# Kernel optimization log

Hardware: AMD Instinct MI355X
Metric: run time of the kernel (lower is better)

## Reference

```python
import jax, jax.numpy as jnp
import numpy as np

N = 100000      # nodes
E = 1600000     # edges (avg degree 16)
EP = 500000     # pos/neg scored edges
DIN, DH, DOUT = 128, 128, 64


def setup_inputs() -> dict:
    key = jax.random.key(0)
    ks = jax.random.split(key, 8)
    x = jax.random.normal(ks[0], (N, DIN), jnp.float32)
    edge_index = jax.random.randint(ks[1], (2, E), 0, N)
    pos_edge_index = jax.random.randint(ks[2], (2, EP), 0, N)
    neg_edge_index = jax.random.randint(ks[3], (2, EP), 0, N)
    s = lambda k, sh: jax.random.normal(k, sh, jnp.float32) * 0.05
    return dict(
        x=x, edge_index=edge_index,
        pos_edge_index=pos_edge_index, neg_edge_index=neg_edge_index,
        W_l0=s(ks[4], (DIN, DH)), b_l0=jnp.zeros((DH,), jnp.float32), W_r0=s(ks[5], (DIN, DH)),
        W_l1=s(ks[6], (DH, DOUT)), b_l1=jnp.zeros((DOUT,), jnp.float32), W_r1=s(ks[7], (DH, DOUT)),
    )


def sage_conv(h, src, dst, W_l, b_l, W_r):
    # PyG SAGEConv (mean aggr): out_i = W_l @ mean_{j in N(i)} h_j + b_l + W_r @ h_i
    msg = h[src]                                                   # [E, d] gather
    agg = jax.ops.segment_sum(msg, dst, num_segments=h.shape[0])   # [N, d]
    deg = jax.ops.segment_sum(jnp.ones((src.shape[0],), h.dtype), dst, num_segments=h.shape[0])
    mean = agg / jnp.maximum(deg, 1.0)[:, None]
    return mean @ W_l + b_l + h @ W_r


def reference(x, edge_index, pos_edge_index, neg_edge_index,
              W_l0, b_l0, W_r0, W_l1, b_l1, W_r1):
    src, dst = edge_index[0], edge_index[1]
    h = sage_conv(x, src, dst, W_l0, b_l0, W_r0)
    h = jax.nn.relu(h)          # dropout is identity in eval mode
    h = sage_conv(h, src, dst, W_l1, b_l1, W_r1)
    pos_scores = (h[pos_edge_index[0]] * h[pos_edge_index[1]]).sum(axis=1)
    neg_scores = (h[neg_edge_index[0]] * h[neg_edge_index[1]]).sum(axis=1)
    return (pos_scores, neg_scores)
```

## Files before the change

kernel.cpp:

```cpp
#include <hip/hip_runtime.h>

#define NN 100000
#define EE 1600000
#define EPE 500000
#define NBINS 196
#define BCAP 12288
#define EPB 2048
#define NB1 782

typedef short bf8_t __attribute__((ext_vector_type(8)));
typedef float f4_t  __attribute__((ext_vector_type(4)));
typedef float f2v  __attribute__((ext_vector_type(2)));

__device__ __forceinline__ unsigned short f2bf(float f) {
    unsigned u = __float_as_uint(f);
    unsigned r = (u + 0x7fffu + ((u >> 16) & 1u)) >> 16;
    return (unsigned short)r;
}
__device__ __forceinline__ float bfl(unsigned u) { return __uint_as_float(u << 16); }
__device__ __forceinline__ float bfh(unsigned u) { return __uint_as_float(u & 0xffff0000u); }

#if __has_builtin(__builtin_amdgcn_cvt_pk_fp8_f32) && __has_builtin(__builtin_amdgcn_cvt_pk_f32_fp8)
__device__ __forceinline__ unsigned pk4_fp8(float a0, float a1, float a2, float a3) {
    int w = 0;
    w = __builtin_amdgcn_cvt_pk_fp8_f32(a0, a1, w, false);
    w = __builtin_amdgcn_cvt_pk_fp8_f32(a2, a3, w, true);
    return (unsigned)w;
}
__device__ __forceinline__ void accf8(float* a, uint2 v) {
    f2v p0 = __builtin_amdgcn_cvt_pk_f32_fp8((int)v.x, false);
    f2v p1 = __builtin_amdgcn_cvt_pk_f32_fp8((int)v.x, true);
    f2v p2 = __builtin_amdgcn_cvt_pk_f32_fp8((int)v.y, false);
    f2v p3 = __builtin_amdgcn_cvt_pk_f32_fp8((int)v.y, true);
    a[0] += p0.x; a[1] += p0.y; a[2] += p1.x; a[3] += p1.y;
    a[4] += p2.x; a[5] += p2.y; a[6] += p3.x; a[7] += p3.y;
}
#else
#include <hip/hip_fp8.h>
__device__ __forceinline__ unsigned pk4_fp8(float a0, float a1, float a2, float a3) {
    unsigned r;
    r  = (unsigned)__hip_cvt_float_to_fp8(a0, __HIP_SATFINITE, __HIP_E4M3);
    r |= (unsigned)__hip_cvt_float_to_fp8(a1, __HIP_SATFINITE, __HIP_E4M3) << 8;
    r |= (unsigned)__hip_cvt_float_to_fp8(a2, __HIP_SATFINITE, __HIP_E4M3) << 16;
    r |= (unsigned)__hip_cvt_float_to_fp8(a3, __HIP_SATFINITE, __HIP_E4M3) << 24;
    return r;
}
__device__ __forceinline__ float dec1_fp8(unsigned b) {
    __hip_fp8_e4m3 h; h.__x = (__hip_fp8_storage_t)(b & 0xff);
    return (float)h;
}
__device__ __forceinline__ void accf8(float* a, uint2 v) {
    a[0] += dec1_fp8(v.x); a[1] += dec1_fp8(v.x >> 8);
    a[2] += dec1_fp8(v.x >> 16); a[3] += dec1_fp8(v.x >> 24);
    a[4] += dec1_fp8(v.y); a[5] += dec1_fp8(v.y >> 8);
    a[6] += dec1_fp8(v.y >> 16); a[7] += dec1_fp8(v.y >> 24);
}
#endif

__global__ __launch_bounds__(256) void binpass1_k(
    const int* __restrict__ src, const int* __restrict__ dst,
    int* __restrict__ bin_cnt, int* __restrict__ binbuf)
{
    __shared__ int cnt_l[NBINS];
    __shared__ int base_l[NBINS];
    int tid = threadIdx.x;
    int e0 = blockIdx.x * EPB;
    for (int i = tid; i < NBINS; i += 256) cnt_l[i] = 0;
    __syncthreads();

    int pk[8];
    #pragma unroll
    for (int i = 0; i < 8; ++i) {
        int e = e0 + tid + i * 256;
        pk[i] = -1;
        if (e < EE) {
            int d = dst[e];
            int b = d >> 9;
            int r = atomicAdd(&cnt_l[b], 1);
            pk[i] = (b << 20) | ((d & 511) << 11) | r;
        }
    }
    __syncthreads();
    for (int i = tid; i < NBINS; i += 256)
        base_l[i] = atomicAdd(&bin_cnt[i], cnt_l[i]);
    __syncthreads();

    #pragma unroll
    for (int i = 0; i < 8; ++i) {
        int e = e0 + tid + i * 256;
        if (e >= EE) continue;
        int v = pk[i];
        int b = v >> 20, dl = (v >> 11) & 511, r = v & 2047;
        binbuf[b * BCAP + base_l[b] + r] = (dl << 17) | src[e];
    }
}

__global__ __launch_bounds__(256) void binpass2_k(
    const int* __restrict__ binbuf, const int* __restrict__ bin_cnt,
    int* __restrict__ csr, int* __restrict__ row_ptr, float* __restrict__ invd)
{
    __shared__ int deg_l[512];
    __shared__ int off_l[512];
    __shared__ int cur_l[512];
    __shared__ int s[256];
    int tid = threadIdx.x;
    int b = blockIdx.x;
    int lo = b << 9;
    int n_here = min(512, NN - lo);

    int bc = (tid < NBINS) ? bin_cnt[tid] : 0;
    s[tid] = bc;
    __syncthreads();
    #pragma unroll
    for (int off = 1; off < 256; off <<= 1) {
        int t = (tid >= off) ? s[tid - off] : 0;
        __syncthreads();
        s[tid] += t;
        __syncthreads();
    }
    int base = (b == 0) ? 0 : s[b - 1];
    int cnt = bin_cnt[b];
    const int* bb = binbuf + b * BCAP;
    __syncthreads();

    deg_l[tid] = 0; deg_l[tid + 256] = 0;
    __syncthreads();
    for (int i = tid; i < cnt; i += 256)
        atomicAdd(&deg_l[bb[i] >> 17], 1);
    __syncthreads();

    int a0 = deg_l[2 * tid], a1 = deg_l[2 * tid + 1];
    s[tid] = a0 + a1;
    __syncthreads();
    #pragma unroll
    for (int off = 1; off < 256; off <<= 1) {
        int t = (tid >= off) ? s[tid - off] : 0;
        __syncthreads();
        s[tid] += t;
        __syncthreads();
    }
    int excl = s[tid] - (a0 + a1);
    off_l[2 * tid] = excl;
    off_l[2 * tid + 1] = excl + a0;
    cur_l[2 * tid] = excl;
    cur_l[2 * tid + 1] = excl + a0;
    __syncthreads();

    for (int j = tid; j < n_here; j += 256) {
        row_ptr[lo + j] = base + off_l[j];
        invd[lo + j] = 1.0f / fmaxf((float)deg_l[j], 1.0f);
    }
    if (tid == 0 && b == NBINS - 1) row_ptr[NN] = EE;

    for (int i = tid; i < cnt; i += 256) {
        int v = bb[i];
        int dstl = v >> 17, srcv = v & 0x1FFFF;
        int pos = atomicAdd(&cur_l[dstl], 1);
        csr[base + pos] = srcv;
    }
}

__global__ void pack_k(const float* __restrict__ Wl0, const float* __restrict__ Wr0,
                       const float* __restrict__ Wl1, const float* __restrict__ Wr1,
                       const float* __restrict__ bl0, const float* __restrict__ bl1,
                       unsigned short* __restrict__ Bp0, unsigned short* __restrict__ Bp1,
                       float* __restrict__ b0p, float* __restrict__ b1p,
                       int* __restrict__ bin_cnt)
{
    int t = blockIdx.x * 256 + threadIdx.x;
    if (t < NBINS) bin_cnt[t] = 0;
    if (t < 4096) {
        int q = t & 3;
        int n = (t >> 2) & 255;
        int kt = t >> 10;
        unsigned short o[8];
        #pragma unroll
        for (int j = 0; j < 8; ++j) {
            int k = kt * 32 + q * 8 + j;
            float v = (n < 128) ? Wl0[(size_t)k * 128 + n] : Wr0[(size_t)k * 128 + (n - 128)];
            o[j] = f2bf(v);
        }
        uint4 w;
        w.x = (unsigned)o[0] | ((unsigned)o[1] << 16);
        w.y = (unsigned)o[2] | ((unsigned)o[3] << 16);
        w.z = (unsigned)o[4] | ((unsigned)o[5] << 16);
        w.w = (unsigned)o[6] | ((unsigned)o[7] << 16);
        *(uint4*)(Bp0 + (size_t)t * 8) = w;
    } else if (t < 6144) {
        int u = t - 4096;
        int q = u & 3;
        int n = (u >> 2) & 127;
        int kt = u >> 9;
        unsigned short o[8];
        #pragma unroll
        for (int j = 0; j < 8; ++j) {
            int k = kt * 32 + q * 8 + j;
            int c = ((k & 7) << 4) | (k >> 3);
            float v = (n < 64) ? Wl1[(size_t)c * 64 + n] : Wr1[(size_t)c * 64 + (n - 64)];
            o[j] = f2bf(v);
        }
        uint4 w;
        w.x = (unsigned)o[0] | ((unsigned)o[1] << 16);
        w.y = (unsigned)o[2] | ((unsigned)o[3] << 16);
        w.z = (unsigned)o[4] | ((unsigned)o[5] << 16);
        w.w = (unsigned)o[6] | ((unsigned)o[7] << 16);
        *(uint4*)(Bp1 + (size_t)u * 8) = w;
    } else if (t < 6144 + 128) {
        int m = t - 6144;
        b0p[m] = bl0[((m & 7) << 4) | (m >> 3)];
    } else if (t < 6144 + 192) {
        int m = t - 6272;
        b1p[m] = bl1[((m & 3) << 4) | (m >> 2)];
    }
}

template<int NCOLS, bool AFP32>
__global__ __launch_bounds__(256) void gemm_k(
    const void* __restrict__ Av, const unsigned short* __restrict__ Bp,
    unsigned char* __restrict__ Tout, unsigned short* __restrict__ Rout)
{
    constexpr int NT = NCOLS / 16;
    constexpr int NTH = NCOLS / 32;
    constexpr int HC = NCOLS / 2;
    int wave = threadIdx.x >> 6;
    int lane = threadIdx.x & 63;
    int ln = lane & 15, q = lane >> 4;
    int row0 = (blockIdx.x * 4 + wave) * 16;
    if (row0 >= NN) return;
    int arow = row0 + ln;

    f4_t acc[NT];
    #pragma unroll
    for (int nt = 0; nt < NT; ++nt) acc[nt] = (f4_t){0.f, 0.f, 0.f, 0.f};

    #pragma unroll
    for (int kt = 0; kt < 4; ++kt) {
        bf8_t a;
        if (AFP32) {
            const float* ap = (const float*)Av + (size_t)arow * 128 + kt * 32 + q * 8;
            f4_t a0 = *(const f4_t*)ap;
            f4_t a1 = *(const f4_t*)(ap + 4);
            #pragma unroll
            for (int j = 0; j < 4; ++j) {
                a[j]     = (short)f2bf(a0[j]);
                a[4 + j] = (short)f2bf(a1[j]);
            }
        } else {
            a = *(const bf8_t*)((const unsigned short*)Av + (size_t)arow * 128 + kt * 32 + q * 8);
        }
        const unsigned short* bb = Bp + (size_t)kt * NCOLS * 32 + (size_t)ln * 32 + q * 8;
        #pragma unroll
        for (int nt = 0; nt < NT; ++nt) {
            bf8_t b = *(const bf8_t*)(bb + nt * 512);
            acc[nt] = __builtin_amdgcn_mfma_f32_16x16x32_bf16(a, b, acc[nt], 0, 0, 0);
        }
    }

    #pragma unroll
    for (int r = 0; r < 4; ++r) {
        int row = row0 + q * 4 + r;
        if (NTH == 8) {
            uint2 wt;
            wt.x = pk4_fp8(acc[0][r], acc[1][r], acc[2][r], acc[3][r]);
            wt.y = pk4_fp8(acc[4][r], acc[5][r], acc[6][r], acc[7][r]);
            *(uint2*)(Tout + (size_t)row * HC + ln * 8) = wt;
            uint4 wr;
            wr.x = (unsigned)f2bf(acc[8][r])  | ((unsigned)f2bf(acc[9][r])  << 16);
            wr.y = (unsigned)f2bf(acc[10][r]) | ((unsigned)f2bf(acc[11][r]) << 16);
            wr.z = (unsigned)f2bf(acc[12][r]) | ((unsigned)f2bf(acc[13][r]) << 16);
            wr.w = (unsigned)f2bf(acc[14][r]) | ((unsigned)f2bf(acc[15][r]) << 16);
            *(uint4*)(Rout + (size_t)row * HC + ln * 8) = wr;
        } else {
            unsigned wt = pk4_fp8(acc[0][r], acc[1][r], acc[2][r], acc[3][r]);
            *(unsigned*)(Tout + (size_t)row * HC + ln * 4) = wt;
            uint2 wr;
            wr.x = (unsigned)f2bf(acc[4][r]) | ((unsigned)f2bf(acc[5][r]) << 16);
            wr.y = (unsigned)f2bf(acc[6][r]) | ((unsigned)f2bf(acc[7][r]) << 16);
            *(uint2*)(Rout + (size_t)row * HC + ln * 4) = wr;
        }
    }
}

__device__ __forceinline__ void unp8(float* a, uint4 v) {
    a[0] = bfl(v.x); a[1] = bfh(v.x);
    a[2] = bfl(v.y); a[3] = bfh(v.y);
    a[4] = bfl(v.z); a[5] = bfh(v.z);
    a[6] = bfl(v.w); a[7] = bfh(v.w);
}

template<int LPNS, bool RELU>
__global__ __launch_bounds__(256) void gather_fuse_k(
    const unsigned char* __restrict__ tq, const int* __restrict__ csr,
    const int* __restrict__ row_ptr, const float* __restrict__ invd,
    const unsigned short* __restrict__ rg, const float* __restrict__ biasp,
    unsigned short* __restrict__ hout)
{
    constexpr int STRIDE = 8 << LPNS;
    int t = blockIdx.x * 256 + threadIdx.x;
    int node = t >> LPNS;
    int lane = t & ((1 << LPNS) - 1);
    if (node >= NN) return;
    int e = row_ptr[node];
    int e1 = row_ptr[node + 1];
    const unsigned char* fb = tq + lane * 8;

    float a0[8] = {0.f, 0.f, 0.f, 0.f, 0.f, 0.f, 0.f, 0.f};
    float a1[8] = {0.f, 0.f, 0.f, 0.f, 0.f, 0.f, 0.f, 0.f};
    for (; e + 3 < e1; e += 4) {
        int s0 = csr[e], s1 = csr[e + 1], s2 = csr[e + 2], s3 = csr[e + 3];
        uint2 v0 = *(const uint2*)(fb + (size_t)s0 * STRIDE);
        uint2 v1 = *(const uint2*)(fb + (size_t)s1 * STRIDE);
        uint2 v2 = *(const uint2*)(fb + (size_t)s2 * STRIDE);
        uint2 v3 = *(const uint2*)(fb + (size_t)s3 * STRIDE);
        accf8(a0, v0); accf8(a1, v1); accf8(a0, v2); accf8(a1, v3);
    }
    for (; e < e1; ++e) {
        int s0 = csr[e];
        uint2 v0 = *(const uint2*)(fb + (size_t)s0 * STRIDE);
        accf8(a0, v0);
    }

    float inv = invd[node];
    uint4 rv = *(const uint4*)(rg + (size_t)node * STRIDE + lane * 8);
    float rr[8];
    unp8(rr, rv);
    f4_t b0 = *(const f4_t*)(biasp + lane * 8);
    f4_t b1 = *(const f4_t*)(biasp + lane * 8 + 4);
    float o[8];
    #pragma unroll
    for (int j = 0; j < 8; ++j) {
        float bj = (j < 4) ? b0[j] : b1[j - 4];
        float v = (a0[j] + a1[j]) * inv + rr[j] + bj;
        o[j] = RELU ? fmaxf(v, 0.f) : v;
    }
    uint4 w;
    w.x = (unsigned)f2bf(o[0]) | ((unsigned)f2bf(o[1]) << 16);
    w.y = (unsigned)f2bf(o[2]) | ((unsigned)f2bf(o[3]) << 16);
    w.z = (unsigned)f2bf(o[4]) | ((unsigned)f2bf(o[5]) << 16);
    w.w = (unsigned)f2bf(o[6]) | ((unsigned)f2bf(o[7]) << 16);
    *(uint4*)(hout + (size_t)node * STRIDE + lane * 8) = w;
}

__device__ __forceinline__ float dot8(uint4 va, uint4 vb) {
    return bfl(va.x) * bfl(vb.x) + bfh(va.x) * bfh(vb.x)
         + bfl(va.y) * bfl(vb.y) + bfh(va.y) * bfh(vb.y)
         + bfl(va.z) * bfl(vb.z) + bfh(va.z) * bfh(vb.z)
         + bfl(va.w) * bfl(vb.w) + bfh(va.w) * bfh(vb.w);
}

__global__ __launch_bounds__(256) void score_k(
    const unsigned short* __restrict__ h2b, const int* __restrict__ pos,
    const int* __restrict__ neg, float* __restrict__ out)
{
    int t = blockIdx.x * 256 + threadIdx.x;
    int g = t >> 3, l = t & 7;
    int eg0 = g * 2;
    if (eg0 >= 2 * EPE) return;
    int eg1 = eg0 + 1;
    int a0i, b0i, a1i, b1i;
    if (eg0 < EPE) { a0i = pos[eg0]; b0i = pos[EPE + eg0]; }
    else { int e2 = eg0 - EPE; a0i = neg[e2]; b0i = neg[EPE + e2]; }
    if (eg1 < EPE) { a1i = pos[eg1]; b1i = pos[EPE + eg1]; }
    else { int e2 = eg1 - EPE; a1i = neg[e2]; b1i = neg[EPE + e2]; }
    const unsigned short* hb = h2b + (size_t)l * 8;
    uint4 va0 = *(const uint4*)(hb + (size_t)a0i * 64);
    uint4 vb0 = *(const uint4*)(hb + (size_t)b0i * 64);
    uint4 va1 = *(const uint4*)(hb + (size_t)a1i * 64);
    uint4 vb1 = *(const uint4*)(hb + (size_t)b1i * 64);
    float p0 = dot8(va0, vb0);
    float p1 = dot8(va1, vb1);
    p0 += __shfl_xor(p0, 1, 8);
    p1 += __shfl_xor(p1, 1, 8);
    p0 += __shfl_xor(p0, 2, 8);
    p1 += __shfl_xor(p1, 2, 8);
    p0 += __shfl_xor(p0, 4, 8);
    p1 += __shfl_xor(p1, 4, 8);
    if (l == 0) { out[eg0] = p0; out[eg1] = p1; }
}

extern "C" void kernel_launch(void* const* d_in, const int* in_sizes, int n_in,
                              void* d_out, int out_size, void* d_ws, size_t ws_size,
                              hipStream_t stream) {
    const float* x   = (const float*)d_in[0];
    const int*   ei  = (const int*)d_in[1];
    const int*   pei = (const int*)d_in[2];
    const int*   nei = (const int*)d_in[3];
    const float* Wl0 = (const float*)d_in[4];
    const float* bl0 = (const float*)d_in[5];
    const float* Wr0 = (const float*)d_in[6];
    const float* Wl1 = (const float*)d_in[7];
    const float* bl1 = (const float*)d_in[8];
    const float* Wr1 = (const float*)d_in[9];
    float* out = (float*)d_out;

    char* ws = (char*)d_ws;
    size_t off = 0;
    auto alloc = [&](size_t bytes) {
        void* p = ws + off;
        off = (off + bytes + 255) & ~(size_t)255;
        return p;
    };
    float* invd     = (float*)alloc((size_t)NN * 4);
    int*   row_ptr  = (int*)  alloc((size_t)(NN + 1) * 4);
    int*   bin_cnt  = (int*)  alloc((size_t)NBINS * 4);
    int*   binbuf   = (int*)  alloc((size_t)NBINS * BCAP * 4);
    int*   csr      = (int*)  alloc((size_t)EE * 4);
    unsigned short* Bp0 = (unsigned short*)alloc((size_t)4096 * 8 * 2);
    unsigned short* Bp1 = (unsigned short*)alloc((size_t)2048 * 8 * 2);
    float* b0p = (float*)alloc(128 * 4);
    float* b1p = (float*)alloc(64 * 4);
    unsigned char*  t0q = (unsigned char*) alloc((size_t)NN * 128);
    unsigned short* r0b = (unsigned short*)alloc((size_t)NN * 128 * 2);
    unsigned short* h1b = (unsigned short*)alloc((size_t)NN * 128 * 2);
    unsigned char*  t1q = t0q;
    unsigned short* r1b = r0b;
    unsigned short* h2b = h1b;

    const int* src = ei;
    const int* dst = ei + EE;

    pack_k<<<25, 256, 0, stream>>>(Wl0, Wr0, Wl1, Wr1, bl0, bl1, Bp0, Bp1, b0p, b1p, bin_cnt);
    binpass1_k<<<NB1, 256, 0, stream>>>(src, dst, bin_cnt, binbuf);
    binpass2_k<<<NBINS, 256, 0, stream>>>(binbuf, bin_cnt, csr, row_ptr, invd);

    gemm_k<256, true><<<1563, 256, 0, stream>>>(x, Bp0, t0q, r0b);
    gather_fuse_k<4, true><<<(NN * 16 + 255) / 256, 256, 0, stream>>>(
        t0q, csr, row_ptr, invd, r0b, b0p, h1b);

    gemm_k<128, false><<<1563, 256, 0, stream>>>(h1b, Bp1, t1q, r1b);
    gather_fuse_k<3, false><<<(NN * 8 + 255) / 256, 256, 0, stream>>>(
        t1q, csr, row_ptr, invd, r1b, b1p, h2b);

    score_k<<<(EPE * 8 + 255) / 256, 256, 0, stream>>>(h2b, pei, nei, out);
}
```

Baseline: 299.0 us.

## Split GEMM columns across waves and keep B fragments in registers

The GEMM now gives each wave a column strip of the output and has it loop over four 16-row tiles, with the B fragments loaded into registers once per block. Before, each wave covered all columns for its own 16 rows and reloaded B for every tile. The column permutation used for the layer-1 weights and the biases is changed to match the new output layout, and a 2-wide fp8 pack is added. In exchange, each A row is now loaded by all four waves instead of one, and the change is only correct if the downstream gather kernel's layout assumptions still hold.

```diff
diff --git a/kernel.cpp b/kernel.cpp
--- a/kernel.cpp
+++ b/kernel.cpp
@@ -20,12 +20,23 @@
 __device__ __forceinline__ float bfl(unsigned u) { return __uint_as_float(u << 16); }
 __device__ __forceinline__ float bfh(unsigned u) { return __uint_as_float(u & 0xffff0000u); }
 
+__device__ __forceinline__ int c0p(int m) {
+    return ((m >> 6) & 1) * 64 + (m & 3) * 16 + ((m >> 2) & 15);
+}
+__device__ __forceinline__ int c1p(int m) {
+    return ((m >> 5) & 1) * 32 + (m & 1) * 16 + ((m >> 1) & 15);
+}
+
 #if __has_builtin(__builtin_amdgcn_cvt_pk_fp8_f32) && __has_builtin(__builtin_amdgcn_cvt_pk_f32_fp8)
 __device__ __forceinline__ unsigned pk4_fp8(float a0, float a1, float a2, float a3) {
     int w = 0;
     w = __builtin_amdgcn_cvt_pk_fp8_f32(a0, a1, w, false);
     w = __builtin_amdgcn_cvt_pk_fp8_f32(a2, a3, w, true);
     return (unsigned)w;
+}
+__device__ __forceinline__ unsigned short pk2_fp8(float a0, float a1) {
+    int w = __builtin_amdgcn_cvt_pk_fp8_f32(a0, a1, 0, false);
+    return (unsigned short)(w & 0xffff);
 }
 __device__ __forceinline__ void accf8(float* a, uint2 v) {
     f2v p0 = __builtin_amdgcn_cvt_pk_f32_fp8((int)v.x, false);
@@ -44,6 +55,12 @@
     r |= (unsigned)__hip_cvt_float_to_fp8(a2, __HIP_SATFINITE, __HIP_E4M3) << 16;
     r |= (unsigned)__hip_cvt_float_to_fp8(a3, __HIP_SATFINITE, __HIP_E4M3) << 24;
     return r;
+}
+__device__ __forceinline__ unsigned short pk2_fp8(float a0, float a1) {
+    unsigned r;
+    r  = (unsigned)__hip_cvt_float_to_fp8(a0, __HIP_SATFINITE, __HIP_E4M3);
+    r |= (unsigned)__hip_cvt_float_to_fp8(a1, __HIP_SATFINITE, __HIP_E4M3) << 8;
+    return (unsigned short)r;
 }
 __device__ __forceinline__ float dec1_fp8(unsigned b) {
     __hip_fp8_e4m3 h; h.__x = (__hip_fp8_storage_t)(b & 0xff);
@@ -195,7 +212,7 @@
         #pragma unroll
         for (int j = 0; j < 8; ++j) {
             int k = kt * 32 + q * 8 + j;
-            int c = ((k & 7) << 4) | (k >> 3);
+            int c = c0p(k);
             float v = (n < 64) ? Wl1[(size_t)c * 64 + n] : Wr1[(size_t)c * 64 + (n - 64)];
             o[j] = f2bf(v);
         }
@@ -207,10 +224,10 @@
         *(uint4*)(Bp1 + (size_t)u * 8) = w;
     } else if (t < 6144 + 128) {
         int m = t - 6144;
-        b0p[m] = bl0[((m & 7) << 4) | (m >> 3)];
+        b0p[m] = bl0[c0p(m)];
     } else if (t < 6144 + 192) {
         int m = t - 6272;
-        b1p[m] = bl1[((m & 3) << 4) | (m >> 2)];
+        b1p[m] = bl1[c1p(m)];
     }
 }
 
@@ -219,64 +236,80 @@
     const void* __restrict__ Av, const unsigned short* __restrict__ Bp,
     unsigned char* __restrict__ Tout, unsigned short* __restrict__ Rout)
 {
-    constexpr int NT = NCOLS / 16;
-    constexpr int NTH = NCOLS / 32;
+    constexpr int STRIP = NCOLS / 4;
+    constexpr int NT = STRIP / 16;
     constexpr int HC = NCOLS / 2;
-    int wave = threadIdx.x >> 6;
+    int w = threadIdx.x >> 6;
     int lane = threadIdx.x & 63;
     int ln = lane & 15, q = lane >> 4;
-    int row0 = (blockIdx.x * 4 + wave) * 16;
-    if (row0 >= NN) return;
-    int arow = row0 + ln;
-
-    f4_t acc[NT];
-    #pragma unroll
-    for (int nt = 0; nt < NT; ++nt) acc[nt] = (f4_t){0.f, 0.f, 0.f, 0.f};
-
-    #pragma unroll
-    for (int kt = 0; kt < 4; ++kt) {
-        bf8_t a;
+    int half = w >> 1, wsub = w & 1;
+    int row0 = blockIdx.x * 64;
+    int colbase = half * HC + wsub * STRIP;
+
+    bf8_t Bf[4][NT];
+    #pragma unroll
+    for (int kt = 0; kt < 4; ++kt)
+        #pragma unroll
+        for (int nt = 0; nt < NT; ++nt)
+            Bf[kt][nt] = *(const bf8_t*)(Bp + (size_t)kt * NCOLS * 32
+                                         + (size_t)(colbase + nt * 16 + ln) * 32 + q * 8);
+
+    for (int rt = 0; rt < 4; ++rt) {
+        int rowt = row0 + rt * 16;
+        if (rowt >= NN) break;
+        int arow = rowt + ln;
+
+        bf8_t Af[4];
         if (AFP32) {
-            const float* ap = (const float*)Av + (size_t)arow * 128 + kt * 32 + q * 8;
-            f4_t a0 = *(const f4_t*)ap;
-            f4_t a1 = *(const f4_t*)(ap + 4);
             #pragma unroll
-            for (int j = 0; j < 4; ++j) {
-                a[j]     = (short)f2bf(a0[j]);
-                a[4 + j] = (short)f2bf(a1[j]);
+            for (int kt = 0; kt < 4; ++kt) {
+                const float* ap = (const float*)Av + (size_t)arow * 128 + kt * 32 + q * 8;
+                f4_t a0 = *(const f4_t*)ap;
+                f4_t a1 = *(const f4_t*)(ap + 4);
+                #pragma unroll
+                for (int j = 0; j < 4; ++j) {
+                    Af[kt][j]     = (short)f2bf(a0[j]);
+                    Af[kt][4 + j] = (short)f2bf(a1[j]);
+                }
             }
         } else {
-            a = *(const bf8_t*)((const unsigned short*)Av + (size_t)arow * 128 + kt * 32 + q * 8);
+            #pragma unroll
+            for (int kt = 0; kt < 4; ++kt)
+                Af[kt] = *(const bf8_t*)((const unsigned short*)Av
+                                         + (size_t)arow * 128 + kt * 32 + q * 8);
         }
-        const unsigned short* bb = Bp + (size_t)kt * NCOLS * 32 + (size_t)ln * 32 + q * 8;
-        #pragma unroll
-        for (int nt = 0; nt < NT; ++nt) {
-            bf8_t b = *(const bf8_t*)(bb + nt * 512);
-            acc[nt] = __builtin_amdgcn_mfma_f32_16x16x32_bf16(a, b, acc[nt], 0, 0, 0);
-        }
-    }
-
-    #pragma unroll
-    for (int r = 0; r < 4; ++r) {
-        int row = row0 + q * 4 + r;
-        if (NTH == 8) {
-            uint2 wt;
-            wt.x = pk4_fp8(acc[0][r], acc[1][r], acc[2][r], acc[3][r]);
-            wt.y = pk4_fp8(acc[4][r], acc[5][r], acc[6][r], acc[7][r]);
-            *(uint2*)(Tout + (size_t)row * HC + ln * 8) = wt;
-            uint4 wr;
-            wr.x = (unsigned)f2bf(acc[8][r])  | ((unsigned)f2bf(acc[9][r])  << 16);
-            wr.y = (unsigned)f2bf(acc[10][r]) | ((unsigned)f2bf(acc[11][r]) << 16);
-            wr.z = (unsigned)f2bf(acc[12][r]) | ((unsigned)f2bf(acc[13][r]) << 16);
-            wr.w = (unsigned)f2bf(acc[14][r]) | ((unsigned)f2bf(acc[15][r]) << 16);
-            *(uint4*)(Rout + (size_t)row * HC + ln * 8) = wr;
-        } else {
-            unsigned wt = pk4_fp8(acc[0][r], acc[1][r], acc[2][r], acc[3][r]);
-            *(unsigned*)(Tout + (size_t)row * HC + ln * 4) = wt;
-            uint2 wr;
-            wr.x = (unsigned)f2bf(acc[4][r]) | ((unsigned)f2bf(acc[5][r]) << 16);
-            wr.y = (unsigned)f2bf(acc[6][r]) | ((unsigned)f2bf(acc[7][r]) << 16);
-            *(uint2*)(Rout + (size_t)row * HC + ln * 4) = wr;
+
+        f4_t acc[NT];
+        #pragma unroll
+        for (int nt = 0; nt < NT; ++nt) acc[nt] = (f4_t){0.f, 0.f, 0.f, 0.f};
+        #pragma unroll
+        for (int kt = 0; kt < 4; ++kt)
+            #pragma unroll
+            for (int nt = 0; nt < NT; ++nt)
+                acc[nt] = __builtin_amdgcn_mfma_f32_16x16x32_bf16(Af[kt], Bf[kt][nt], acc[nt], 0, 0, 0);
+
+        #pragma unroll
+        for (int r = 0; r < 4; ++r) {
+            int row = rowt + q * 4 + r;
+            if (half == 0) {
+                if (NT == 4) {
+                    unsigned v = pk4_fp8(acc[0][r], acc[1][r], acc[2][r], acc[3][r]);
+                    *(unsigned*)(Tout + (size_t)row * HC + wsub * 64 + ln * 4) = v;
+                } else {
+                    unsigned short v = pk2_fp8(acc[0][r], acc[1][r]);
+                    *(unsigned short*)(Tout + (size_t)row * HC + wsub * 32 + ln * 2) = v;
+                }
+            } else {
+                if (NT == 4) {
+                    uint2 v;
+                    v.x = (unsigned)f2bf(acc[0][r]) | ((unsigned)f2bf(acc[1][r]) << 16);
+                    v.y = (unsigned)f2bf(acc[2][r]) | ((unsigned)f2bf(acc[3][r]) << 16);
+                    *(uint2*)(Rout + (size_t)row * HC + wsub * 64 + ln * 4) = v;
+                } else {
+                    unsigned v = (unsigned)f2bf(acc[0][r]) | ((unsigned)f2bf(acc[1][r]) << 16);
+                    *(unsigned*)(Rout + (size_t)row * HC + wsub * 32 + ln * 2) = v;
+                }
+            }
         }
     }
 }
```

Measured after the change: 297.9 us. No clear change (-0.4%).
